# Optimization experiments

Hardware: AMD Instinct MI355X
Metric: run time of the kernel (lower is better)

## Reference

```python
import jax, jax.numpy as jnp
import numpy as np

N = 50000       # nodes
E = 800000      # edges
QD = 128        # q_dim == k_dim == v_dim
PD = 64         # pair_dim
H = 8           # num_heads
HD = 16         # head_dim (H*HD == QD)


def setup_inputs() -> dict:
    key = jax.random.key(0)
    ks = jax.random.split(key, 12)
    s = 0.05  # small init scale for weights
    return {
        "q": jax.random.normal(ks[0], (N, QD), jnp.float32),
        "k": jax.random.normal(ks[1], (N, QD), jnp.float32),
        "v": jax.random.normal(ks[2], (N, QD), jnp.float32),
        "edges": jax.random.normal(ks[3], (E, PD), jnp.float32),
        "edge_index": jax.random.randint(ks[4], (E, 2), 0, N, dtype=jnp.int32),
        # learned parameters (stored [in, out]; x @ W == torch Linear)
        "Wq": jax.random.normal(ks[5], (QD, H * HD), jnp.float32) * s,
        "Wk": jax.random.normal(ks[6], (QD, H * HD), jnp.float32) * s,
        "Wv": jax.random.normal(ks[7], (QD, H * HD), jnp.float32) * s,
        "Wo": jax.random.normal(ks[8], (H * HD, QD), jnp.float32) * s,
        "bo": jnp.zeros((QD,), jnp.float32),
        "Wb": jax.random.normal(ks[9], (PD, H), jnp.float32) * s,
        "bb": jnp.zeros((H,), jnp.float32),
    }


def reference(q, k, v, edges, edge_index, Wq, Wk, Wv, Wo, bo, Wb, bb):
    n_node = q.shape[0]
    # projections + head split; q pre-scaled by head_dim**-0.5 (as in torch code)
    qh = (q @ Wq).reshape(n_node, H, HD) * (HD ** -0.5)   # [N,H,HD]
    kh = (k @ Wk).reshape(n_node, H, HD)
    vh = (v @ Wv).reshape(n_node, H, HD)
    dst = edge_index[:, 0]
    src = edge_index[:, 1]
    qe = qh[dst]                                           # [E,H,HD] gather
    ke = kh[src]
    ve = vh[src]
    # per-edge, per-head attention logits + learned pair bias
    attn = jnp.einsum('ehd,ehd->eh', qe, ke) + edges @ Wb + bb  # [E,H]
    # scatter_softmax over destination-node segments
    m = jax.ops.segment_max(attn, dst, num_segments=n_node)      # [N,H]
    ex = jnp.exp(attn - m[dst])
    den = jax.ops.segment_sum(ex, dst, num_segments=n_node)      # [N,H]
    p = ex / den[dst]                                            # [E,H]
    # weighted value aggregation back to nodes
    o = jax.ops.segment_sum(p[:, :, None] * ve, dst, num_segments=n_node)  # [N,H,HD]
    o = o.reshape(n_node, H * HD)
    return o @ Wo + bo
```

## Files before the change

### kernel.cpp

```cpp
#include <hip/hip_runtime.h>
#include <hip/hip_bf16.h>
#include <math.h>

#define NN 50000
#define EE 800000

__global__ __launch_bounds__(256) void gemm128_k(
    const float* __restrict__ A, const float* __restrict__ W,
    const float* __restrict__ bias, float* __restrict__ C,
    int n_rows, float scale) {
  __shared__ float Al[64 * 132];
  const int t = threadIdx.x;
  const int row0 = blockIdx.x * 64;
  for (int i = t; i < 64 * 32; i += 256) {
    int r = i >> 5, c4 = i & 31;
    int gr = row0 + r;
    float4 val = make_float4(0.f, 0.f, 0.f, 0.f);
    if (gr < n_rows) val = *(const float4*)&A[(size_t)gr * 128 + c4 * 4];
    *(float4*)&Al[r * 132 + c4 * 4] = val;
  }
  __syncthreads();
  const int tx = t & 31;
  const int ty = t >> 5;
  float acc[8][4] = {};
  #pragma unroll 8
  for (int k = 0; k < 128; ++k) {
    float4 w = *(const float4*)&W[k * 128 + tx * 4];
    #pragma unroll
    for (int r = 0; r < 8; ++r) {
      float a = Al[(ty * 8 + r) * 132 + k];
      acc[r][0] = fmaf(a, w.x, acc[r][0]);
      acc[r][1] = fmaf(a, w.y, acc[r][1]);
      acc[r][2] = fmaf(a, w.z, acc[r][2]);
      acc[r][3] = fmaf(a, w.w, acc[r][3]);
    }
  }
  float4 bv = make_float4(0.f, 0.f, 0.f, 0.f);
  if (bias) bv = *(const float4*)&bias[tx * 4];
  #pragma unroll
  for (int r = 0; r < 8; ++r) {
    int gr = row0 + ty * 8 + r;
    if (gr < n_rows) {
      float4 o;
      o.x = acc[r][0] * scale + bv.x;
      o.y = acc[r][1] * scale + bv.y;
      o.z = acc[r][2] * scale + bv.z;
      o.w = acc[r][3] * scale + bv.w;
      *(float4*)&C[(size_t)gr * 128 + tx * 4] = o;
    }
  }
}

__global__ __launch_bounds__(256) void edge_attn_k(
    const float* __restrict__ qh, const float* __restrict__ kh,
    const float* __restrict__ edges, const float* __restrict__ Wb,
    const float* __restrict__ bb, const int* __restrict__ eidx,
    float* __restrict__ attn) {
  __shared__ float Wbl[64 * 8];
  __shared__ float bbl[8];
  for (int i = threadIdx.x; i < 64 * 8; i += 256) Wbl[i] = Wb[i];
  if (threadIdx.x < 8) bbl[threadIdx.x] = bb[threadIdx.x];
  __syncthreads();
  int gid = blockIdx.x * 256 + threadIdx.x;
  int e = gid >> 3, h = gid & 7;
  if (e >= EE) return;
  int dst = eidx[2 * e + 0];
  int src = eidx[2 * e + 1];
  const float4* qv = (const float4*)&qh[(size_t)dst * 128 + h * 16];
  const float4* kv = (const float4*)&kh[(size_t)src * 128 + h * 16];
  float s = 0.f;
  #pragma unroll
  for (int i = 0; i < 4; ++i) {
    float4 a = qv[i], b = kv[i];
    s = fmaf(a.x, b.x, s); s = fmaf(a.y, b.y, s);
    s = fmaf(a.z, b.z, s); s = fmaf(a.w, b.w, s);
  }
  const float4* ev = (const float4*)&edges[(size_t)e * 64];
  float bsum = bbl[h];
  #pragma unroll
  for (int p4 = 0; p4 < 16; ++p4) {
    float4 ee = ev[p4];
    bsum = fmaf(ee.x, Wbl[(p4 * 4 + 0) * 8 + h], bsum);
    bsum = fmaf(ee.y, Wbl[(p4 * 4 + 1) * 8 + h], bsum);
    bsum = fmaf(ee.z, Wbl[(p4 * 4 + 2) * 8 + h], bsum);
    bsum = fmaf(ee.w, Wbl[(p4 * 4 + 3) * 8 + h], bsum);
  }
  attn[(size_t)e * 8 + h] = s + bsum;
}

__global__ __launch_bounds__(256) void count_k(const int* __restrict__ eidx,
                                               int* __restrict__ counts) {
  int e = blockIdx.x * 256 + threadIdx.x;
  if (e < EE) atomicAdd(&counts[eidx[2 * e]], 1);
}

__global__ __launch_bounds__(1024) void scan_k(const int* __restrict__ counts,
                                               int* __restrict__ offs,
                                               int* __restrict__ cursor) {
  __shared__ int sd[1024];
  int t = threadIdx.x;
  int carry = 0;
  for (int base = 0; base < NN; base += 1024) {
    int idx = base + t;
    int val = (idx < NN) ? counts[idx] : 0;
    sd[t] = val;
    __syncthreads();
    for (int off = 1; off < 1024; off <<= 1) {
      int x = (t >= off) ? sd[t - off] : 0;
      __syncthreads();
      sd[t] += x;
      __syncthreads();
    }
    int excl = carry + sd[t] - val;
    if (idx < NN) { offs[idx] = excl; cursor[idx] = excl; }
    carry += sd[1023];
    __syncthreads();
  }
  if (t == 0) offs[NN] = carry;
}

__global__ __launch_bounds__(256) void scatter_k(const int* __restrict__ eidx,
                                                 int* __restrict__ cursor,
                                                 int* __restrict__ elist) {
  int e = blockIdx.x * 256 + threadIdx.x;
  if (e < EE) {
    int pos = atomicAdd(&cursor[eidx[2 * e]], 1);
    elist[pos] = e;
  }
}

__global__ __launch_bounds__(256) void aggregate_k(
    const float* __restrict__ attn, const float* __restrict__ vh,
    const int* __restrict__ eidx, const int* __restrict__ offs,
    const int* __restrict__ elist, float* __restrict__ o) {
  int wid = (blockIdx.x * 256 + threadIdx.x) >> 6;
  int lane = threadIdx.x & 63;
  if (wid >= NN) return;
  int beg = offs[wid], end = offs[wid + 1];
  int h = lane >> 3;
  int d = lane * 2;
  float m = -INFINITY;
  for (int i = beg; i < end; ++i) {
    int e = elist[i];
    m = fmaxf(m, attn[(size_t)e * 8 + h]);
  }
  float den = 0.f, acc0 = 0.f, acc1 = 0.f;
  for (int i = beg; i < end; ++i) {
    int e = elist[i];
    float a = attn[(size_t)e * 8 + h];
    int src = eidx[2 * e + 1];
    float ex = __expf(a - m);
    den += ex;
    float2 vv = *(const float2*)&vh[(size_t)src * 128 + d];
    acc0 = fmaf(ex, vv.x, acc0);
    acc1 = fmaf(ex, vv.y, acc1);
  }
  float2 r;
  if (end > beg) { r.x = acc0 / den; r.y = acc1 / den; }
  else           { r.x = 0.f; r.y = 0.f; }
  *(float2*)&o[(size_t)wid * 128 + d] = r;
}

extern "C" void kernel_launch(void* const* d_in, const int* in_sizes, int n_in,
                              void* d_out, int out_size, void* d_ws, size_t ws_size,
                              hipStream_t stream) {
  const float* q     = (const float*)d_in[0];
  const float* k     = (const float*)d_in[1];
  const float* v     = (const float*)d_in[2];
  const float* edges = (const float*)d_in[3];
  const int*   eidx  = (const int*)  d_in[4];
  const float* Wq    = (const float*)d_in[5];
  const float* Wk    = (const float*)d_in[6];
  const float* Wv    = (const float*)d_in[7];
  const float* Wo    = (const float*)d_in[8];
  const float* bo    = (const float*)d_in[9];
  const float* Wb    = (const float*)d_in[10];
  const float* bb    = (const float*)d_in[11];
  float* out = (float*)d_out;

  char* ws = (char*)d_ws;
  float* qh   = (float*)ws; ws += (size_t)NN * 128 * 4;
  float* kh   = (float*)ws; ws += (size_t)NN * 128 * 4;
  float* vh   = (float*)ws; ws += (size_t)NN * 128 * 4;
  float* attn = (float*)ws; ws += (size_t)EE * 8 * 4;
  int* counts = (int*)ws;   ws += (size_t)NN * 4;
  int* offs   = (int*)ws;   ws += (size_t)(NN + 1) * 4;
  int* cursor = (int*)ws;   ws += (size_t)NN * 4;
  int* elist  = (int*)ws;   ws += (size_t)EE * 4;
  float* obuf = qh;

  hipMemsetAsync(counts, 0, (size_t)NN * 4, stream);

  const int gemm_grid = (NN + 63) / 64;
  gemm128_k<<<gemm_grid, 256, 0, stream>>>(q, Wq, nullptr, qh, NN, 0.25f);
  gemm128_k<<<gemm_grid, 256, 0, stream>>>(k, Wk, nullptr, kh, NN, 1.0f);
  gemm128_k<<<gemm_grid, 256, 0, stream>>>(v, Wv, nullptr, vh, NN, 1.0f);

  count_k  <<<(EE + 255) / 256, 256, 0, stream>>>(eidx, counts);
  scan_k   <<<1, 1024, 0, stream>>>(counts, offs, cursor);
  scatter_k<<<(EE + 255) / 256, 256, 0, stream>>>(eidx, cursor, elist);

  edge_attn_k<<<(EE * 8 + 255) / 256, 256, 0, stream>>>(qh, kh, edges, Wb, bb, eidx, attn);

  aggregate_k<<<(NN * 64 + 255) / 256, 256, 0, stream>>>(attn, vh, eidx, offs, elist, obuf);

  gemm128_k<<<gemm_grid, 256, 0, stream>>>(obuf, Wo, bo, out, NN, 1.0f);
}
```

Baseline: 901.5 us.

## Parallelize CSR scan and compute edge attention in destination-sorted order

Replaces the single-block serial scan with a two-pass multi-block scan (per-block partial sums, then per-block prefix plus a base offset). The scatter kernel now also writes dst and src per sorted position. Edge attention is computed in CSR order and stored by position, so aggregation reads attention contiguously and no longer chases elist or eidx. In exchange, the edges rows and the k-head gathers in edge_attn become indirect and scattered, and two extra index arrays are written.

New measurement: 762.2 us. 1.18x faster.

```diff
diff --git a/kernel.cpp b/kernel.cpp
--- a/kernel.cpp
+++ b/kernel.cpp
@@ -4,6 +4,7 @@
 
 #define NN 50000
 #define EE 800000
+#define NBLK 49
 
 __global__ __launch_bounds__(256) void gemm128_k(
     const float* __restrict__ A, const float* __restrict__ W,
@@ -51,21 +52,90 @@
   }
 }
 
+__global__ __launch_bounds__(256) void count_k(const int* __restrict__ eidx,
+                                               int* __restrict__ counts) {
+  int e = blockIdx.x * 256 + threadIdx.x;
+  if (e < EE) atomicAdd(&counts[eidx[2 * e]], 1);
+}
+
+__global__ __launch_bounds__(256) void partial_k(const int* __restrict__ counts,
+                                                 int* __restrict__ partials) {
+  __shared__ int sd[256];
+  int b = blockIdx.x, t = threadIdx.x;
+  int sum = 0;
+  for (int i = t; i < 1024; i += 256) {
+    int idx = b * 1024 + i;
+    sum += (idx < NN) ? counts[idx] : 0;
+  }
+  sd[t] = sum;
+  __syncthreads();
+  for (int off = 128; off > 0; off >>= 1) {
+    if (t < off) sd[t] += sd[t + off];
+    __syncthreads();
+  }
+  if (t == 0) partials[b] = sd[0];
+}
+
+__global__ __launch_bounds__(1024) void offs_k(const int* __restrict__ counts,
+                                               const int* __restrict__ partials,
+                                               int* __restrict__ offs,
+                                               int* __restrict__ cursor) {
+  __shared__ int sd[1024];
+  int b = blockIdx.x, t = threadIdx.x;
+  int idx = b * 1024 + t;
+  int val = (idx < NN) ? counts[idx] : 0;
+  sd[t] = val;
+  __syncthreads();
+  for (int off = 1; off < 1024; off <<= 1) {
+    int x = (t >= off) ? sd[t - off] : 0;
+    __syncthreads();
+    sd[t] += x;
+    __syncthreads();
+  }
+  int base = 0;
+  for (int j = 0; j < b; ++j) base += partials[j];
+  int excl = base + sd[t] - val;
+  if (idx < NN) { offs[idx] = excl; cursor[idx] = excl; }
+  if (b == 0 && t == 0) {
+    int tot = 0;
+    for (int j = 0; j < NBLK; ++j) tot += partials[j];
+    offs[NN] = tot;
+  }
+}
+
+__global__ __launch_bounds__(256) void scatter_k(const int* __restrict__ eidx,
+                                                 int* __restrict__ cursor,
+                                                 int* __restrict__ elist,
+                                                 int* __restrict__ dstp,
+                                                 int* __restrict__ srcp) {
+  int e = blockIdx.x * 256 + threadIdx.x;
+  if (e < EE) {
+    int dst = eidx[2 * e + 0];
+    int src = eidx[2 * e + 1];
+    int pos = atomicAdd(&cursor[dst], 1);
+    elist[pos] = e;
+    dstp[pos] = dst;
+    srcp[pos] = src;
+  }
+}
+
 __global__ __launch_bounds__(256) void edge_attn_k(
     const float* __restrict__ qh, const float* __restrict__ kh,
     const float* __restrict__ edges, const float* __restrict__ Wb,
-    const float* __restrict__ bb, const int* __restrict__ eidx,
-    float* __restrict__ attn) {
+    const float* __restrict__ bb, const int* __restrict__ elist,
+    const int* __restrict__ dstp, const int* __restrict__ srcp,
+    float* __restrict__ attnp) {
   __shared__ float Wbl[64 * 8];
   __shared__ float bbl[8];
   for (int i = threadIdx.x; i < 64 * 8; i += 256) Wbl[i] = Wb[i];
   if (threadIdx.x < 8) bbl[threadIdx.x] = bb[threadIdx.x];
   __syncthreads();
   int gid = blockIdx.x * 256 + threadIdx.x;
-  int e = gid >> 3, h = gid & 7;
-  if (e >= EE) return;
-  int dst = eidx[2 * e + 0];
-  int src = eidx[2 * e + 1];
+  int pos = gid >> 3, h = gid & 7;
+  if (pos >= EE) return;
+  int e   = elist[pos];
+  int dst = dstp[pos];
+  int src = srcp[pos];
   const float4* qv = (const float4*)&qh[(size_t)dst * 128 + h * 16];
   const float4* kv = (const float4*)&kh[(size_t)src * 128 + h * 16];
   float s = 0.f;
@@ -85,54 +155,13 @@
     bsum = fmaf(ee.z, Wbl[(p4 * 4 + 2) * 8 + h], bsum);
     bsum = fmaf(ee.w, Wbl[(p4 * 4 + 3) * 8 + h], bsum);
   }
-  attn[(size_t)e * 8 + h] = s + bsum;
-}
-
-__global__ __launch_bounds__(256) void count_k(const int* __restrict__ eidx,
-                                               int* __restrict__ counts) {
-  int e = blockIdx.x * 256 + threadIdx.x;
-  if (e < EE) atomicAdd(&counts[eidx[2 * e]], 1);
-}
-
-__global__ __launch_bounds__(1024) void scan_k(const int* __restrict__ counts,
-                                               int* __restrict__ offs,
-                                               int* __restrict__ cursor) {
-  __shared__ int sd[1024];
-  int t = threadIdx.x;
-  int carry = 0;
-  for (int base = 0; base < NN; base += 1024) {
-    int idx = base + t;
-    int val = (idx < NN) ? counts[idx] : 0;
-    sd[t] = val;
-    __syncthreads();
-    for (int off = 1; off < 1024; off <<= 1) {
-      int x = (t >= off) ? sd[t - off] : 0;
-      __syncthreads();
-      sd[t] += x;
-      __syncthreads();
-    }
-    int excl = carry + sd[t] - val;
-    if (idx < NN) { offs[idx] = excl; cursor[idx] = excl; }
-    carry += sd[1023];
-    __syncthreads();
-  }
-  if (t == 0) offs[NN] = carry;
-}
-
-__global__ __launch_bounds__(256) void scatter_k(const int* __restrict__ eidx,
-                                                 int* __restrict__ cursor,
-                                                 int* __restrict__ elist) {
-  int e = blockIdx.x * 256 + threadIdx.x;
-  if (e < EE) {
-    int pos = atomicAdd(&cursor[eidx[2 * e]], 1);
-    elist[pos] = e;
-  }
+  attnp[(size_t)pos * 8 + h] = s + bsum;
 }
 
 __global__ __launch_bounds__(256) void aggregate_k(
-    const float* __restrict__ attn, const float* __restrict__ vh,
-    const int* __restrict__ eidx, const int* __restrict__ offs,
-    const int* __restrict__ elist, float* __restrict__ o) {
+    const float* __restrict__ attnp, const float* __restrict__ vh,
+    const int* __restrict__ srcp, const int* __restrict__ offs,
+    float* __restrict__ o) {
   int wid = (blockIdx.x * 256 + threadIdx.x) >> 6;
   int lane = threadIdx.x & 63;
   if (wid >= NN) return;
@@ -140,15 +169,12 @@
   int h = lane >> 3;
   int d = lane * 2;
   float m = -INFINITY;
-  for (int i = beg; i < end; ++i) {
-    int e = elist[i];
-    m = fmaxf(m, attn[(size_t)e * 8 + h]);
-  }
+  for (int i = beg; i < end; ++i)
+    m = fmaxf(m, attnp[(size_t)i * 8 + h]);
   float den = 0.f, acc0 = 0.f, acc1 = 0.f;
   for (int i = beg; i < end; ++i) {
-    int e = elist[i];
-    float a = attn[(size_t)e * 8 + h];
-    int src = eidx[2 * e + 1];
+    float a = attnp[(size_t)i * 8 + h];
+    int src = srcp[i];
     float ex = __expf(a - m);
     den += ex;
     float2 vv = *(const float2*)&vh[(size_t)src * 128 + d];
@@ -179,14 +205,17 @@
   float* out = (float*)d_out;
 
   char* ws = (char*)d_ws;
-  float* qh   = (float*)ws; ws += (size_t)NN * 128 * 4;
-  float* kh   = (float*)ws; ws += (size_t)NN * 128 * 4;
-  float* vh   = (float*)ws; ws += (size_t)NN * 128 * 4;
-  float* attn = (float*)ws; ws += (size_t)EE * 8 * 4;
-  int* counts = (int*)ws;   ws += (size_t)NN * 4;
-  int* offs   = (int*)ws;   ws += (size_t)(NN + 1) * 4;
-  int* cursor = (int*)ws;   ws += (size_t)NN * 4;
-  int* elist  = (int*)ws;   ws += (size_t)EE * 4;
+  float* qh    = (float*)ws; ws += (size_t)NN * 128 * 4;
+  float* kh    = (float*)ws; ws += (size_t)NN * 128 * 4;
+  float* vh    = (float*)ws; ws += (size_t)NN * 128 * 4;
+  float* attnp = (float*)ws; ws += (size_t)EE * 8 * 4;
+  int* counts  = (int*)ws;   ws += (size_t)NN * 4;
+  int* offs    = (int*)ws;   ws += (size_t)(NN + 1) * 4;
+  int* cursor  = (int*)ws;   ws += (size_t)NN * 4;
+  int* partials= (int*)ws;   ws += (size_t)64 * 4;
+  int* elist   = (int*)ws;   ws += (size_t)EE * 4;
+  int* dstp    = (int*)ws;   ws += (size_t)EE * 4;
+  int* srcp    = (int*)ws;   ws += (size_t)EE * 4;
   float* obuf = qh;
 
   hipMemsetAsync(counts, 0, (size_t)NN * 4, stream);
@@ -197,12 +226,14 @@
   gemm128_k<<<gemm_grid, 256, 0, stream>>>(v, Wv, nullptr, vh, NN, 1.0f);
 
   count_k  <<<(EE + 255) / 256, 256, 0, stream>>>(eidx, counts);
-  scan_k   <<<1, 1024, 0, stream>>>(counts, offs, cursor);
-  scatter_k<<<(EE + 255) / 256, 256, 0, stream>>>(eidx, cursor, elist);
-
-  edge_attn_k<<<(EE * 8 + 255) / 256, 256, 0, stream>>>(qh, kh, edges, Wb, bb, eidx, attn);
-
-  aggregate_k<<<(NN * 64 + 255) / 256, 256, 0, stream>>>(attn, vh, eidx, offs, elist, obuf);
+  partial_k<<<NBLK, 256, 0, stream>>>(counts, partials);
+  offs_k   <<<NBLK, 1024, 0, stream>>>(counts, partials, offs, cursor);
+  scatter_k<<<(EE + 255) / 256, 256, 0, stream>>>(eidx, cursor, elist, dstp, srcp);
+
+  edge_attn_k<<<(EE * 8 + 255) / 256, 256, 0, stream>>>(qh, kh, edges, Wb, bb,
+                                                        elist, dstp, srcp, attnp);
+
+  aggregate_k<<<(NN * 64 + 255) / 256, 256, 0, stream>>>(attnp, vh, srcp, offs, obuf);
 
   gemm128_k<<<gemm_grid, 256, 0, stream>>>(obuf, Wo, bo, out, NN, 1.0f);
 }
```
